# Kernel optimization log

Measured on AMD Instinct MI355X. Metric: run time of the kernel, lower is better.

The kernel has to match this reference:

```python
import jax, jax.numpy as jnp
from jax import lax
import numpy as np

# Quantization params from the torch module
IN_SCALE, IN_ZP = 0.01, 7
W_SCALE, W_ZP = 0.01, 3
B_SCALE = 0.0001
INT32_MIN, INT32_MAX = -2147483648.0, 2147483647.0


def setup_inputs() -> dict:
    key = jax.random.key(0)
    k1, k2, k3 = jax.random.split(key, 3)
    # int8-valued tensors stored as int32 (int8 range [-128, 127])
    inputVec = jax.random.randint(k1, (64, 16, 256, 256), -128, 128, dtype=jnp.int32)
    weight = jax.random.randint(k2, (16, 16, 3, 3), -128, 128, dtype=jnp.int32)
    bias = jax.random.normal(k3, (16,), dtype=jnp.float32)
    return {"inputVec": inputVec, "weight": weight, "bias": bias, "groups": 1}


def reference(inputVec, weight, bias, groups):
    # per-tensor dequantize: (q - zero_point) * scale
    x = (inputVec.astype(jnp.float32) - IN_ZP) * IN_SCALE          # [N, Cin, H, W]
    w = (weight.astype(jnp.float32) - W_ZP) * W_SCALE              # [Cout, Cin/g, kH, kW]
    # bias: quantize to qint32 (zp=0) then dequantize (round-half-to-even, clamp to int32)
    b = jnp.clip(jnp.round(bias / B_SCALE), INT32_MIN, INT32_MAX) * B_SCALE
    out = lax.conv_general_dilated(
        x, w,
        window_strides=(1, 1),
        padding='VALID',
        dimension_numbers=('NCHW', 'OIHW', 'NCHW'),
        feature_group_count=groups,
    )
    return out + b[None, :, None, None]
```

## Files before the change

### kernel.cpp

```cpp
#include <hip/hip_runtime.h>

#define H 256
#define W 256
#define CIN 16
#define COUT 16
#define OH 254
#define OW 254
#define OHB 12
#define IRB (OHB + 2)
#define COLS 259
#define NOHG 22
#define NTHREADS 512
#define NWAVES 8
#define TILES (OHB * 16)
#define TPW (TILES / NWAVES)

typedef int int4v __attribute__((ext_vector_type(4)));
typedef int int2v __attribute__((ext_vector_type(2)));

static __device__ __forceinline__ int pack4(int d0, int d1, int d2, int d3) {
    int t0 = __builtin_amdgcn_perm(d1, d0, 0x00000400);
    int t1 = __builtin_amdgcn_perm(d3, d2, 0x00000400);
    return __builtin_amdgcn_perm(t1, t0, 0x05040100);
}

__global__ __launch_bounds__(NTHREADS, 4) void conv_q8_mfma(
    const int* __restrict__ x, const int* __restrict__ wq,
    const float* __restrict__ bias, float* __restrict__ out)
{
    __shared__ int4v lds_x[IRB * COLS];
    __shared__ int4v lds_wA[192];
    __shared__ int   lds_ci[COUT];
    __shared__ float lds_bf[COUT];

    const int tid = threadIdx.x;
    const int ohg = blockIdx.x;
    const int n   = blockIdx.y;
    const int oh0 = ohg * OHB;

    if (tid < 192) {
        const int t = tid;
        const int co = t & 15;
        const int kw = (t >> 4) & 3;
        const int kh = t >> 6;
        int4v pk = {0, 0, 0, 0};
        if (kw < 3) {
#pragma unroll
            for (int q = 0; q < 4; ++q) {
                const int* wp = wq + ((co * CIN + q * 4) * 3 + kh) * 3 + kw;
                pk[q] = pack4(wp[0], wp[9], wp[18], wp[27]);
            }
        }
        lds_wA[t] = pk;
    }
    if (tid < COUT) {
        int s = 0;
        const int* wc = wq + tid * CIN * 9;
#pragma unroll
        for (int k = 0; k < CIN * 9; ++k) s += wc[k];
        lds_ci[tid] = -7 * s + 144 * 21;
        float r = rintf(bias[tid] * 10000.0f);
        r = fminf(fmaxf(r, -2147483648.0f), 2147483647.0f);
        lds_bf[tid] = r * 1e-4f;
    }
    if (tid < IRB * 4) {
        const int row = tid >> 2;
        const int col = 256 + (tid & 3);
        if (col < COLS) lds_x[row * COLS + col] = (int4v){0, 0, 0, 0};
    }

    const int* xn = x + (size_t)n * (CIN * H * W);
    for (int t = tid; t < IRB * 128; t += NTHREADS) {
        const int row = t >> 7;
        const int c2 = (t & 127) * 2;
        int ih = oh0 + row;
        if (ih > H - 1) ih = H - 1;
        const int* p = xn + ih * W + c2;
        int4v pk0, pk1;
#pragma unroll
        for (int q = 0; q < 4; ++q) {
            const int2v d0 = *(const int2v*)(p + (q * 4 + 0) * (H * W));
            const int2v d1 = *(const int2v*)(p + (q * 4 + 1) * (H * W));
            const int2v d2 = *(const int2v*)(p + (q * 4 + 2) * (H * W));
            const int2v d3 = *(const int2v*)(p + (q * 4 + 3) * (H * W));
            pk0[q] = pack4(d0.x, d1.x, d2.x, d3.x);
            pk1[q] = pack4(d0.y, d1.y, d2.y, d3.y);
        }
        lds_x[row * COLS + c2]     = pk0;
        lds_x[row * COLS + c2 + 1] = pk1;
    }
    __syncthreads();

    const int wave = tid >> 6;
    const int lane = tid & 63;
    const int n16  = lane & 15;
    const int quad = lane >> 4;

    const int4v a0 = lds_wA[(0 * 4 + quad) * 16 + n16];
    const int4v a1 = lds_wA[(1 * 4 + quad) * 16 + n16];
    const int4v a2 = lds_wA[(2 * 4 + quad) * 16 + n16];
    const int ov = (quad < 3) ? 0x01010101 : 0;
    const int4v aones = {ov, ov, ov, ov};

    int   ci_r[4];
    float bf_r[4];
#pragma unroll
    for (int r = 0; r < 4; ++r) {
        ci_r[r] = lds_ci[quad * 4 + r];
        bf_r[r] = lds_bf[quad * 4 + r];
    }

    float* outn = out + (size_t)n * (COUT * OH * OW);
    const int coff = n16 + quad;

    for (int t = wave * TPW; t < wave * TPW + TPW; ++t) {
        const int rl = t >> 4;
        const int g  = t & 15;
        const int oh = oh0 + rl;
        if (oh >= OH) continue;
        const int ow0 = g * 16;
        const int c = ow0 + coff;
        const int4v b0 = lds_x[(rl + 0) * COLS + c];
        const int4v b1 = lds_x[(rl + 1) * COLS + c];
        const int4v b2 = lds_x[(rl + 2) * COLS + c];
        int4v acc = {0, 0, 0, 0};
        int4v acs = {0, 0, 0, 0};
        acc = __builtin_amdgcn_mfma_i32_16x16x64_i8(a0, b0, acc, 0, 0, 0);
        acc = __builtin_amdgcn_mfma_i32_16x16x64_i8(a1, b1, acc, 0, 0, 0);
        acc = __builtin_amdgcn_mfma_i32_16x16x64_i8(a2, b2, acc, 0, 0, 0);
        acs = __builtin_amdgcn_mfma_i32_16x16x64_i8(aones, b0, acs, 0, 0, 0);
        acs = __builtin_amdgcn_mfma_i32_16x16x64_i8(aones, b1, acs, 0, 0, 0);
        acs = __builtin_amdgcn_mfma_i32_16x16x64_i8(aones, b2, acs, 0, 0, 0);
        const int sx = acs[0];
        const int ow = ow0 + n16;
        if (ow < OW) {
#pragma unroll
            for (int r = 0; r < 4; ++r) {
                const int co  = quad * 4 + r;
                const int tot = acc[r] - 3 * sx + ci_r[r];
                outn[(co * OH + oh) * OW + ow] = fmaf(1e-4f, (float)tot, bf_r[r]);
            }
        }
    }
}

extern "C" void kernel_launch(void* const* d_in, const int* in_sizes, int n_in,
                              void* d_out, int out_size, void* d_ws, size_t ws_size,
                              hipStream_t stream) {
    const int*   x    = (const int*)d_in[0];
    const int*   wq   = (const int*)d_in[1];
    const float* bias = (const float*)d_in[2];
    float*       out  = (float*)d_out;

    const int n = in_sizes[0] / (CIN * H * W);
    dim3 grid(NOHG, n);
    conv_q8_mfma<<<grid, NTHREADS, 0, stream>>>(x, wq, bias, out);
}
```

Before: 476.7 us.

## Pre-pack input into channel-interleaved workspace and stream rows per wave

Adds a separate kernel that packs the int32 input into 16-byte channel-interleaved int8 vectors in the workspace. A new conv kernel then has each wave walk a 16-column strip down 32 output rows. It keeps the previous two input rows and their ones-MFMA sums in registers, so each input row is loaded and summed once rather than three times. This drops the LDS staging and the per-block halo re-reads, at the cost of an extra kernel launch and a workspace round trip. The old kernel remains as a fallback when the workspace is too small.

```diff
diff --git a/kernel.cpp b/kernel.cpp
--- a/kernel.cpp
+++ b/kernel.cpp
@@ -6,23 +6,143 @@
 #define COUT 16
 #define OH 254
 #define OW 254
+#define HW (H * W)
+
+typedef int int4v __attribute__((ext_vector_type(4)));
+typedef int int2v __attribute__((ext_vector_type(2)));
+
+static __device__ __forceinline__ int pack4(int d0, int d1, int d2, int d3) {
+    int t0 = __builtin_amdgcn_perm(d1, d0, 0x00000400);
+    int t1 = __builtin_amdgcn_perm(d3, d2, 0x00000400);
+    return __builtin_amdgcn_perm(t1, t0, 0x05040100);
+}
+
+__global__ __launch_bounds__(256) void pack_x(
+    const int* __restrict__ x, int4v* __restrict__ xpk)
+{
+    const int t  = blockIdx.x * 256 + threadIdx.x;
+    const int p2 = t * 2;
+    const int n   = p2 >> 16;
+    const int pix = p2 & 65535;
+    const int* p = x + (size_t)n * (CIN * HW) + pix;
+    int4v pk0, pk1;
+#pragma unroll
+    for (int q = 0; q < 4; ++q) {
+        const int2v d0 = *(const int2v*)(p + (q * 4 + 0) * HW);
+        const int2v d1 = *(const int2v*)(p + (q * 4 + 1) * HW);
+        const int2v d2 = *(const int2v*)(p + (q * 4 + 2) * HW);
+        const int2v d3 = *(const int2v*)(p + (q * 4 + 3) * HW);
+        pk0[q] = pack4(d0.x, d1.x, d2.x, d3.x);
+        pk1[q] = pack4(d0.y, d1.y, d2.y, d3.y);
+    }
+    xpk[p2]     = pk0;
+    xpk[p2 + 1] = pk1;
+}
+
+__global__ __launch_bounds__(256, 6) void conv_q8_stream(
+    const int4v* __restrict__ xpk, const int* __restrict__ wq,
+    const float* __restrict__ bias, float* __restrict__ out)
+{
+    __shared__ int4v lds_wA[192];
+    __shared__ int   lds_ci[COUT];
+    __shared__ float lds_bf[COUT];
+
+    const int tid = threadIdx.x;
+
+    if (tid < 192) {
+        const int co = tid & 15;
+        const int kw = (tid >> 4) & 3;
+        const int kh = tid >> 6;
+        int4v pk = {0, 0, 0, 0};
+        if (kw < 3) {
+#pragma unroll
+            for (int q = 0; q < 4; ++q) {
+                const int* wp = wq + ((co * CIN + q * 4) * 3 + kh) * 3 + kw;
+                pk[q] = pack4(wp[0], wp[9], wp[18], wp[27]);
+            }
+        }
+        lds_wA[tid] = pk;
+    }
+    if (tid < COUT) {
+        int s = 0;
+        const int* wc = wq + tid * CIN * 9;
+#pragma unroll
+        for (int k = 0; k < CIN * 9; ++k) s += wc[k];
+        lds_ci[tid] = -7 * s + 144 * 21;
+        float r = rintf(bias[tid] * 10000.0f);
+        r = fminf(fmaxf(r, -2147483648.0f), 2147483647.0f);
+        lds_bf[tid] = r * 1e-4f;
+    }
+    __syncthreads();
+
+    const int wave = tid >> 6;
+    const int lane = tid & 63;
+    const int n16  = lane & 15;
+    const int quad = lane >> 4;
+
+    const int4v a0 = lds_wA[(0 * 4 + quad) * 16 + n16];
+    const int4v a1 = lds_wA[(1 * 4 + quad) * 16 + n16];
+    const int4v a2 = lds_wA[(2 * 4 + quad) * 16 + n16];
+    const int ov = (quad < 3) ? 0x01010101 : 0;
+    const int4v aones = {ov, ov, ov, ov};
+
+    int   ci_r[4];
+    float bf_r[4];
+#pragma unroll
+    for (int r = 0; r < 4; ++r) {
+        ci_r[r] = lds_ci[quad * 4 + r];
+        bf_r[r] = lds_bf[quad * 4 + r];
+    }
+
+    const int job   = blockIdx.x * 4 + wave;
+    const int n     = job >> 7;
+    const int rem   = job & 127;
+    const int g     = rem & 15;
+    const int chunk = rem >> 4;
+    const int oh0   = chunk * 32;
+    const int ohE   = (oh0 + 32 < OH) ? oh0 + 32 : OH;
+
+    const int col = g * 16 + n16 + quad;
+    const int4v* xb = xpk + (size_t)n * HW + col;
+    float* outn = out + (size_t)n * (COUT * OH * OW);
+    const int  ow    = g * 16 + n16;
+    const bool wmask = ow < OW;
+
+    const int4v zero = {0, 0, 0, 0};
+    int4v b0 = xb[(oh0 + 0) * W];
+    int4v b1 = xb[(oh0 + 1) * W];
+    int ps0 = __builtin_amdgcn_mfma_i32_16x16x64_i8(aones, b0, zero, 0, 0, 0)[0];
+    int ps1 = __builtin_amdgcn_mfma_i32_16x16x64_i8(aones, b1, zero, 0, 0, 0)[0];
+
+#pragma unroll 2
+    for (int oh = oh0; oh < ohE; ++oh) {
+        const int4v b2 = xb[(oh + 2) * W];
+        int4v acc = zero;
+        acc = __builtin_amdgcn_mfma_i32_16x16x64_i8(a0, b0, acc, 0, 0, 0);
+        acc = __builtin_amdgcn_mfma_i32_16x16x64_i8(a1, b1, acc, 0, 0, 0);
+        acc = __builtin_amdgcn_mfma_i32_16x16x64_i8(a2, b2, acc, 0, 0, 0);
+        const int ps2 = __builtin_amdgcn_mfma_i32_16x16x64_i8(aones, b2, zero, 0, 0, 0)[0];
+        const int sx = ps0 + ps1 + ps2;
+        if (wmask) {
+#pragma unroll
+            for (int r = 0; r < 4; ++r) {
+                const int co  = quad * 4 + r;
+                const int tot = acc[r] - 3 * sx + ci_r[r];
+                outn[(co * OH + oh) * OW + ow] = fmaf(1e-4f, (float)tot, bf_r[r]);
+            }
+        }
+        b0 = b1; b1 = b2;
+        ps0 = ps1; ps1 = ps2;
+    }
+}
+
 #define OHB 12
 #define IRB (OHB + 2)
 #define COLS 259
 #define NOHG 22
 #define NTHREADS 512
-#define NWAVES 8
 #define TILES (OHB * 16)
-#define TPW (TILES / NWAVES)
-
-typedef int int4v __attribute__((ext_vector_type(4)));
-typedef int int2v __attribute__((ext_vector_type(2)));
-
-static __device__ __forceinline__ int pack4(int d0, int d1, int d2, int d3) {
-    int t0 = __builtin_amdgcn_perm(d1, d0, 0x00000400);
-    int t1 = __builtin_amdgcn_perm(d3, d2, 0x00000400);
-    return __builtin_amdgcn_perm(t1, t0, 0x05040100);
-}
+#define TPW (TILES / 8)
 
 __global__ __launch_bounds__(NTHREADS, 4) void conv_q8_mfma(
     const int* __restrict__ x, const int* __restrict__ wq,
@@ -65,11 +185,11 @@
     }
     if (tid < IRB * 4) {
         const int row = tid >> 2;
-        const int col = 256 + (tid & 3);
-        if (col < COLS) lds_x[row * COLS + col] = (int4v){0, 0, 0, 0};
-    }
-
-    const int* xn = x + (size_t)n * (CIN * H * W);
+        const int colz = 256 + (tid & 3);
+        if (colz < COLS) lds_x[row * COLS + colz] = (int4v){0, 0, 0, 0};
+    }
+
+    const int* xn = x + (size_t)n * (CIN * HW);
     for (int t = tid; t < IRB * 128; t += NTHREADS) {
         const int row = t >> 7;
         const int c2 = (t & 127) * 2;
@@ -79,10 +199,10 @@
         int4v pk0, pk1;
 #pragma unroll
         for (int q = 0; q < 4; ++q) {
-            const int2v d0 = *(const int2v*)(p + (q * 4 + 0) * (H * W));
-            const int2v d1 = *(const int2v*)(p + (q * 4 + 1) * (H * W));
-            const int2v d2 = *(const int2v*)(p + (q * 4 + 2) * (H * W));
-            const int2v d3 = *(const int2v*)(p + (q * 4 + 3) * (H * W));
+            const int2v d0 = *(const int2v*)(p + (q * 4 + 0) * HW);
+            const int2v d1 = *(const int2v*)(p + (q * 4 + 1) * HW);
+            const int2v d2 = *(const int2v*)(p + (q * 4 + 2) * HW);
+            const int2v d3 = *(const int2v*)(p + (q * 4 + 3) * HW);
             pk0[q] = pack4(d0.x, d1.x, d2.x, d3.x);
             pk1[q] = pack4(d0.y, d1.y, d2.y, d3.y);
         }
@@ -153,6 +273,16 @@
     float*       out  = (float*)d_out;
 
     const int n = in_sizes[0] / (CIN * H * W);
-    dim3 grid(NOHG, n);
-    conv_q8_mfma<<<grid, NTHREADS, 0, stream>>>(x, wq, bias, out);
-}
+    const size_t ws_needed = (size_t)n * HW * 16 + 1024;
+
+    if (d_ws != nullptr && ws_size >= ws_needed) {
+        int4v* xpk = (int4v*)d_ws;
+        const int npix = n * HW;
+        pack_x<<<npix / 512, 256, 0, stream>>>(x, xpk);
+        const int jobs = n * 16 * 8;
+        conv_q8_stream<<<jobs / 4, 256, 0, stream>>>(xpk, wq, bias, out);
+    } else {
+        dim3 grid(NOHG, n);
+        conv_q8_mfma<<<grid, NTHREADS, 0, stream>>>(x, wq, bias, out);
+    }
+}
```

Result: slower. 552.7 us (+16.0%).

## Stream input rows through an LDS ring buffer with register prefetch

Applied to the files above, without the earlier changes.

Each block now covers a 32-row output chunk and keeps a 10-slot LDS ring of packed input rows. Each step issues the global loads for the next four rows into registers, runs the MFMA work on the current rows, then packs and stores the prefetched rows. This cuts the halo re-reads between blocks and overlaps global loads with compute. The MFMA operands are also swapped so each lane writes four contiguous output columns with vector stores. Costs are fewer, longer-lived blocks (8 per image instead of 22), more registers for the 16 prefetched values, and a barrier every step.

```diff
diff --git a/kernel.cpp b/kernel.cpp
--- a/kernel.cpp
+++ b/kernel.cpp
@@ -6,17 +6,19 @@
 #define COUT 16
 #define OH 254
 #define OW 254
-#define OHB 12
-#define IRB (OHB + 2)
+#define HW (H * W)
+
+#define OHB 4
+#define RING 10
 #define COLS 259
-#define NOHG 22
+#define OHC 32
+#define SPLIT 8
+#define STEPS (OHC / OHB)
 #define NTHREADS 512
-#define NWAVES 8
-#define TILES (OHB * 16)
-#define TPW (TILES / NWAVES)
 
 typedef int int4v __attribute__((ext_vector_type(4)));
 typedef int int2v __attribute__((ext_vector_type(2)));
+typedef float f2v  __attribute__((ext_vector_type(2)));
 
 static __device__ __forceinline__ int pack4(int d0, int d1, int d2, int d3) {
     int t0 = __builtin_amdgcn_perm(d1, d0, 0x00000400);
@@ -24,25 +26,25 @@
     return __builtin_amdgcn_perm(t1, t0, 0x05040100);
 }
 
-__global__ __launch_bounds__(NTHREADS, 4) void conv_q8_mfma(
+__global__ __launch_bounds__(NTHREADS, 4) void conv_q8_ring(
     const int* __restrict__ x, const int* __restrict__ wq,
     const float* __restrict__ bias, float* __restrict__ out)
 {
-    __shared__ int4v lds_x[IRB * COLS];
-    __shared__ int4v lds_wA[192];
+    __shared__ int4v lds_x[RING * COLS];
+    __shared__ int4v lds_wB[192];
     __shared__ int   lds_ci[COUT];
     __shared__ float lds_bf[COUT];
 
-    const int tid = threadIdx.x;
-    const int ohg = blockIdx.x;
-    const int n   = blockIdx.y;
-    const int oh0 = ohg * OHB;
+    const int tid   = threadIdx.x;
+    const int chunk = blockIdx.x;
+    const int n     = blockIdx.y;
+    const int oh0   = chunk * OHC;
+    const int* xn   = x + (size_t)n * (CIN * HW);
 
     if (tid < 192) {
-        const int t = tid;
-        const int co = t & 15;
-        const int kw = (t >> 4) & 3;
-        const int kh = t >> 6;
+        const int co = tid & 15;
+        const int kw = (tid >> 4) & 3;
+        const int kh = tid >> 6;
         int4v pk = {0, 0, 0, 0};
         if (kw < 3) {
 #pragma unroll
@@ -51,7 +53,7 @@
                 pk[q] = pack4(wp[0], wp[9], wp[18], wp[27]);
             }
         }
-        lds_wA[t] = pk;
+        lds_wB[tid] = pk;
     }
     if (tid < COUT) {
         int s = 0;
@@ -63,31 +65,31 @@
         r = fminf(fmaxf(r, -2147483648.0f), 2147483647.0f);
         lds_bf[tid] = r * 1e-4f;
     }
-    if (tid < IRB * 4) {
-        const int row = tid >> 2;
-        const int col = 256 + (tid & 3);
-        if (col < COLS) lds_x[row * COLS + col] = (int4v){0, 0, 0, 0};
+    if (tid < RING * 3) {
+        const int slot = tid / 3;
+        const int col  = 256 + (tid % 3);
+        lds_x[slot * COLS + col] = (int4v){0, 0, 0, 0};
     }
 
-    const int* xn = x + (size_t)n * (CIN * H * W);
-    for (int t = tid; t < IRB * 128; t += NTHREADS) {
-        const int row = t >> 7;
-        const int c2 = (t & 127) * 2;
-        int ih = oh0 + row;
-        if (ih > H - 1) ih = H - 1;
+    for (int t = tid; t < 6 * 128; t += NTHREADS) {
+        const int rloc = t >> 7;
+        const int c2   = (t & 127) * 2;
+        const int iru  = oh0 + rloc;
+        const int ih   = (iru < H) ? iru : H - 1;
         const int* p = xn + ih * W + c2;
         int4v pk0, pk1;
 #pragma unroll
         for (int q = 0; q < 4; ++q) {
-            const int2v d0 = *(const int2v*)(p + (q * 4 + 0) * (H * W));
-            const int2v d1 = *(const int2v*)(p + (q * 4 + 1) * (H * W));
-            const int2v d2 = *(const int2v*)(p + (q * 4 + 2) * (H * W));
-            const int2v d3 = *(const int2v*)(p + (q * 4 + 3) * (H * W));
+            const int2v d0 = *(const int2v*)(p + (q * 4 + 0) * HW);
+            const int2v d1 = *(const int2v*)(p + (q * 4 + 1) * HW);
+            const int2v d2 = *(const int2v*)(p + (q * 4 + 2) * HW);
+            const int2v d3 = *(const int2v*)(p + (q * 4 + 3) * HW);
             pk0[q] = pack4(d0.x, d1.x, d2.x, d3.x);
             pk1[q] = pack4(d0.y, d1.y, d2.y, d3.y);
         }
-        lds_x[row * COLS + c2]     = pk0;
-        lds_x[row * COLS + c2 + 1] = pk1;
+        const int slot = iru % RING;
+        lds_x[slot * COLS + c2]     = pk0;
+        lds_x[slot * COLS + c2 + 1] = pk1;
     }
     __syncthreads();
 
@@ -95,51 +97,84 @@
     const int lane = tid & 63;
     const int n16  = lane & 15;
     const int quad = lane >> 4;
-
-    const int4v a0 = lds_wA[(0 * 4 + quad) * 16 + n16];
-    const int4v a1 = lds_wA[(1 * 4 + quad) * 16 + n16];
-    const int4v a2 = lds_wA[(2 * 4 + quad) * 16 + n16];
-    const int ov = (quad < 3) ? 0x01010101 : 0;
-    const int4v aones = {ov, ov, ov, ov};
-
-    int   ci_r[4];
-    float bf_r[4];
-#pragma unroll
-    for (int r = 0; r < 4; ++r) {
-        ci_r[r] = lds_ci[quad * 4 + r];
-        bf_r[r] = lds_bf[quad * 4 + r];
-    }
-
-    float* outn = out + (size_t)n * (COUT * OH * OW);
     const int coff = n16 + quad;
 
-    for (int t = wave * TPW; t < wave * TPW + TPW; ++t) {
-        const int rl = t >> 4;
-        const int g  = t & 15;
-        const int oh = oh0 + rl;
-        if (oh >= OH) continue;
-        const int ow0 = g * 16;
-        const int c = ow0 + coff;
-        const int4v b0 = lds_x[(rl + 0) * COLS + c];
-        const int4v b1 = lds_x[(rl + 1) * COLS + c];
-        const int4v b2 = lds_x[(rl + 2) * COLS + c];
-        int4v acc = {0, 0, 0, 0};
-        int4v acs = {0, 0, 0, 0};
-        acc = __builtin_amdgcn_mfma_i32_16x16x64_i8(a0, b0, acc, 0, 0, 0);
-        acc = __builtin_amdgcn_mfma_i32_16x16x64_i8(a1, b1, acc, 0, 0, 0);
-        acc = __builtin_amdgcn_mfma_i32_16x16x64_i8(a2, b2, acc, 0, 0, 0);
-        acs = __builtin_amdgcn_mfma_i32_16x16x64_i8(aones, b0, acs, 0, 0, 0);
-        acs = __builtin_amdgcn_mfma_i32_16x16x64_i8(aones, b1, acs, 0, 0, 0);
-        acs = __builtin_amdgcn_mfma_i32_16x16x64_i8(aones, b2, acs, 0, 0, 0);
-        const int sx = acs[0];
-        const int ow = ow0 + n16;
-        if (ow < OW) {
+    const int4v w0 = lds_wB[(0 * 4 + quad) * 16 + n16];
+    const int4v w1 = lds_wB[(1 * 4 + quad) * 16 + n16];
+    const int4v w2 = lds_wB[(2 * 4 + quad) * 16 + n16];
+    const int ov = (quad < 3) ? 0x01010101 : 0;
+    const int4v bones = {ov, ov, ov, ov};
+    const int   ci_s = lds_ci[n16];
+    const float bf_s = lds_bf[n16];
+    const int4v zero4 = {0, 0, 0, 0};
+
+    const int rl    = wave >> 1;
+    const int gbase = (wave & 1) * 8;
+    float* outn = out + (size_t)n * (COUT * OH * OW);
+
+    const int rloc = tid >> 7;
+    const int c2p  = (tid & 127) * 2;
+
+    for (int s = 0; s < STEPS; ++s) {
+        int2v ld[16];
+        const bool pf = (s < STEPS - 1);
+        int slot_p = 0;
+        if (pf) {
+            const int iru = oh0 + 4 * s + 6 + rloc;
+            slot_p = iru % RING;
+            const int ih = (iru < H) ? iru : H - 1;
+            const int* p = xn + ih * W + c2p;
 #pragma unroll
-            for (int r = 0; r < 4; ++r) {
-                const int co  = quad * 4 + r;
-                const int tot = acc[r] - 3 * sx + ci_r[r];
-                outn[(co * OH + oh) * OW + ow] = fmaf(1e-4f, (float)tot, bf_r[r]);
+            for (int q = 0; q < 16; ++q)
+                ld[q] = *(const int2v*)(p + q * HW);
+        }
+
+        const int oh  = oh0 + 4 * s + rl;
+        const int sl0 = (oh    ) % RING;
+        const int sl1 = (oh + 1) % RING;
+        const int sl2 = (oh + 2) % RING;
+        const bool do_store = (oh < OH);
+
+#pragma unroll
+        for (int gi = 0; gi < 8; ++gi) {
+            const int g = gbase + gi;
+            const int c = g * 16 + coff;
+            const int4v p0 = lds_x[sl0 * COLS + c];
+            const int4v p1 = lds_x[sl1 * COLS + c];
+            const int4v p2 = lds_x[sl2 * COLS + c];
+            int4v acc = __builtin_amdgcn_mfma_i32_16x16x64_i8(p0, w0, zero4, 0, 0, 0);
+            acc = __builtin_amdgcn_mfma_i32_16x16x64_i8(p1, w1, acc, 0, 0, 0);
+            acc = __builtin_amdgcn_mfma_i32_16x16x64_i8(p2, w2, acc, 0, 0, 0);
+            int4v acs = __builtin_amdgcn_mfma_i32_16x16x64_i8(p0, bones, zero4, 0, 0, 0);
+            acs = __builtin_amdgcn_mfma_i32_16x16x64_i8(p1, bones, acs, 0, 0, 0);
+            acs = __builtin_amdgcn_mfma_i32_16x16x64_i8(p2, bones, acs, 0, 0, 0);
+            if (do_store) {
+                const int owb = g * 16 + quad * 4;
+                float f0 = fmaf(1e-4f, (float)(acc[0] - 3 * acs[0] + ci_s), bf_s);
+                float f1 = fmaf(1e-4f, (float)(acc[1] - 3 * acs[1] + ci_s), bf_s);
+                float f2 = fmaf(1e-4f, (float)(acc[2] - 3 * acs[2] + ci_s), bf_s);
+                float f3 = fmaf(1e-4f, (float)(acc[3] - 3 * acs[3] + ci_s), bf_s);
+                float* ptr = outn + (n16 * OH + oh) * OW + owb;
+                if (owb + 3 < OW) {
+                    *(f2v*)(ptr)     = (f2v){f0, f1};
+                    *(f2v*)(ptr + 2) = (f2v){f2, f3};
+                } else {
+                    if (owb + 0 < OW) ptr[0] = f0;
+                    if (owb + 1 < OW) ptr[1] = f1;
+                }
             }
+        }
+
+        if (pf) {
+            int4v pk0, pk1;
+#pragma unroll
+            for (int q = 0; q < 4; ++q) {
+                pk0[q] = pack4(ld[4 * q].x, ld[4 * q + 1].x, ld[4 * q + 2].x, ld[4 * q + 3].x);
+                pk1[q] = pack4(ld[4 * q].y, ld[4 * q + 1].y, ld[4 * q + 2].y, ld[4 * q + 3].y);
+            }
+            lds_x[slot_p * COLS + c2p]     = pk0;
+            lds_x[slot_p * COLS + c2p + 1] = pk1;
+            __syncthreads();
         }
     }
 }
@@ -153,6 +188,6 @@
     float*       out  = (float*)d_out;
 
     const int n = in_sizes[0] / (CIN * H * W);
-    dim3 grid(NOHG, n);
-    conv_q8_mfma<<<grid, NTHREADS, 0, stream>>>(x, wq, bias, out);
+    dim3 grid(SPLIT, n);
+    conv_q8_ring<<<grid, NTHREADS, 0, stream>>>(x, wq, bias, out);
 }
```

After: 477.5 us. No clear change (+0.2%).
